# Optimization experiments

Measured on AMD Instinct MI355X. Metric: run time of the kernel, lower is better.

Reference implementation:

```python
import jax, jax.numpy as jnp
import numpy as np

N = 100000      # nodes
E = 3200000     # edges (before self-loops)
IN = 1          # input feature dim
H1, C = 4, 8    # layer1: 4 heads x 8 channels; layer2: 1 head x 8 channels
NEG_SLOPE = 0.2


def setup_inputs() -> dict:
    key = jax.random.key(0)
    ks = jax.random.split(key, 10)
    x = jax.random.normal(ks[0], (N, IN), jnp.float32)
    edge_index = jax.random.randint(ks[1], (2, E), 0, N, dtype=jnp.int32)
    # layer 1 params (GATConv(1, 8, heads=4))
    W1 = jax.random.normal(ks[2], (IN, H1 * C), jnp.float32) * 0.5
    a_src1 = jax.random.normal(ks[3], (H1, C), jnp.float32) * 0.5
    a_dst1 = jax.random.normal(ks[4], (H1, C), jnp.float32) * 0.5
    b1 = jnp.zeros((H1 * C,), jnp.float32)
    # layer 2 params (GATConv(32, 8, heads=1))
    W2 = jax.random.normal(ks[5], (H1 * C, C), jnp.float32) * 0.2
    a_src2 = jax.random.normal(ks[6], (1, C), jnp.float32) * 0.5
    a_dst2 = jax.random.normal(ks[7], (1, C), jnp.float32) * 0.5
    b2 = jnp.zeros((C,), jnp.float32)
    return {"x": x, "edge_index": edge_index, "W1": W1, "a_src1": a_src1,
            "a_dst1": a_dst1, "b1": b1, "W2": W2, "a_src2": a_src2,
            "a_dst2": a_dst2, "b2": b2}


def _gat_layer(x, src, dst, W, a_s, a_d, b, heads, ch):
    # Linear transform per head: [N, heads, ch]
    h = (x @ W).reshape(-1, heads, ch)
    # per-node attention logits
    al_s = jnp.einsum('nhc,hc->nh', h, a_s)  # [N, H]
    al_d = jnp.einsum('nhc,hc->nh', h, a_d)  # [N, H]
    # per-edge logits (message src -> dst)
    e = jax.nn.leaky_relu(al_s[src] + al_d[dst], NEG_SLOPE)  # [E', H]
    # segment softmax over incoming edges of each dst node
    m = jax.ops.segment_max(e, dst, num_segments=N)          # [N, H]
    e = jnp.exp(e - m[dst])
    s = jax.ops.segment_sum(e, dst, num_segments=N)          # [N, H]
    alpha = e / s[dst]                                       # [E', H]
    # weighted scatter-add aggregation
    out = jax.ops.segment_sum(h[src] * alpha[:, :, None], dst, num_segments=N)
    return out.reshape(N, heads * ch) + b


def reference(x, edge_index, W1, a_src1, a_dst1, b1, W2, a_src2, a_dst2, b2):
    loops = jnp.arange(N, dtype=edge_index.dtype)
    src = jnp.concatenate([edge_index[0], loops])  # add self-loops (PyG default)
    dst = jnp.concatenate([edge_index[1], loops])
    h = _gat_layer(x, src, dst, W1, a_src1, a_dst1, b1, H1, C)
    h = jax.nn.relu(h)
    out = _gat_layer(h, src, dst, W2, a_src2, a_dst2, b2, 1, C)
    return out
```

## Files before the change

kernel.cpp:

```cpp
#include <hip/hip_runtime.h>
#include <hip/hip_bf16.h>

#define NEG_SLOPE 0.2f
#define CAP   6144
#define CAPG  8192
#define CAPA  81920


__global__ void init_cc(int* __restrict__ curA, int* __restrict__ curB,
                        const float* __restrict__ W1,
                        const float* __restrict__ as1,
                        const float* __restrict__ ad1,
                        float* __restrict__ consts) {
    int t = threadIdx.x;
    if (t < 8) {
        int h = t & 3;
        const float* a = (t < 4) ? as1 : ad1;
        float s = 0.f;
        #pragma unroll
        for (int c = 0; c < 8; ++c)
            s += W1[h * 8 + c] * a[h * 8 + c];
        consts[t] = s;
    }
    if (t < 64) curA[t] = t * CAPA;
    curB[t] = t << 13;
}

__global__ void scatterA(const int* __restrict__ ei, int* __restrict__ curA,
                         unsigned int* __restrict__ bufA, int E) {
    __shared__ int cnt[64];
    __shared__ int basel[64];
    int t = threadIdx.x;
    int chunk = (E + gridDim.x - 1) / gridDim.x;
    int lo = blockIdx.x * chunk;
    int hi = min(E, lo + chunk);
    const int* dei = ei + E;
    if (t < 64) cnt[t] = 0;
    __syncthreads();
    bool vec = ((E & 3) == 0);
    int lo4 = (lo + 3) & ~3;
    int end4 = hi & ~3;
    if (vec && end4 > lo4) {
        for (int e = lo + t; e < lo4; e += 1024)
            atomicAdd(&cnt[dei[e] >> 11], 1);
        const int4* dei4 = (const int4*)dei;
        for (int v = (lo4 >> 2) + t; v < (end4 >> 2); v += 1024) {
            int4 d = dei4[v];
            atomicAdd(&cnt[d.x >> 11], 1);
            atomicAdd(&cnt[d.y >> 11], 1);
            atomicAdd(&cnt[d.z >> 11], 1);
            atomicAdd(&cnt[d.w >> 11], 1);
        }
        for (int e = end4 + t; e < hi; e += 1024)
            atomicAdd(&cnt[dei[e] >> 11], 1);
    } else {
        for (int e = lo + t; e < hi; e += 1024)
            atomicAdd(&cnt[dei[e] >> 11], 1);
    }
    __syncthreads();
    if (t < 64) {
        int c = cnt[t];
        basel[t] = c ? (atomicAdd(&curA[t], c) - t * CAPA) : 0;
        cnt[t] = 0;
    }
    __syncthreads();
    if (vec && end4 > lo4) {
        for (int e = lo + t; e < lo4; e += 1024) {
            int s = ei[e], d = dei[e];
            int sp = d >> 11;
            int off = basel[sp] + atomicAdd(&cnt[sp], 1);
            if (off < CAPA) bufA[sp * CAPA + off] = (unsigned)s | ((unsigned)(d & 2047) << 17);
        }
        const int4* sei4 = (const int4*)ei;
        const int4* dei4 = (const int4*)dei;
        for (int v = (lo4 >> 2) + t; v < (end4 >> 2); v += 1024) {
            int4 sv = sei4[v];
            int4 dv = dei4[v];
            int s0 = dv.x >> 11, s1 = dv.y >> 11, s2 = dv.z >> 11, s3 = dv.w >> 11;
            int o0 = basel[s0] + atomicAdd(&cnt[s0], 1);
            if (o0 < CAPA) bufA[s0 * CAPA + o0] = (unsigned)sv.x | ((unsigned)(dv.x & 2047) << 17);
            int o1 = basel[s1] + atomicAdd(&cnt[s1], 1);
            if (o1 < CAPA) bufA[s1 * CAPA + o1] = (unsigned)sv.y | ((unsigned)(dv.y & 2047) << 17);
            int o2 = basel[s2] + atomicAdd(&cnt[s2], 1);
            if (o2 < CAPA) bufA[s2 * CAPA + o2] = (unsigned)sv.z | ((unsigned)(dv.z & 2047) << 17);
            int o3 = basel[s3] + atomicAdd(&cnt[s3], 1);
            if (o3 < CAPA) bufA[s3 * CAPA + o3] = (unsigned)sv.w | ((unsigned)(dv.w & 2047) << 17);
        }
        for (int e = end4 + t; e < hi; e += 1024) {
            int s = ei[e], d = dei[e];
            int sp = d >> 11;
            int off = basel[sp] + atomicAdd(&cnt[sp], 1);
            if (off < CAPA) bufA[sp * CAPA + off] = (unsigned)s | ((unsigned)(d & 2047) << 17);
        }
    } else {
        for (int e = lo + t; e < hi; e += 1024) {
            int s = ei[e], d = dei[e];
            int sp = d >> 11;
            int off = basel[sp] + atomicAdd(&cnt[sp], 1);
            if (off < CAPA) bufA[sp * CAPA + off] = (unsigned)s | ((unsigned)(d & 2047) << 17);
        }
    }
}

__global__ void scatterB(const int* __restrict__ curA, int* __restrict__ curB,
                         const unsigned int* __restrict__ bufA,
                         unsigned int* __restrict__ pairs) {
    __shared__ int cnt[16];
    __shared__ int basel[16];
    int t = threadIdx.x;
    int sp = blockIdx.x >> 3;
    int part = blockIdx.x & 7;
    int base = sp * CAPA;
    int fill = min(curA[sp] - base, CAPA);
    if (fill <= 0) return;
    int lo = (fill * part) >> 3;
    int hi = (fill * (part + 1)) >> 3;
    for (int c0 = lo; c0 < hi; c0 += 8192) {
        int cend = min(hi, c0 + 8192);
        if (t < 16) cnt[t] = 0;
        __syncthreads();
        for (int i = c0 + t; i < cend; i += 1024)
            atomicAdd(&cnt[(bufA[base + i] >> 24) & 15], 1);
        __syncthreads();
        if (t < 16) {
            int c = cnt[t];
            int bkg = (sp << 4) + t;
            basel[t] = c ? (atomicAdd(&curB[bkg], c) - (bkg << 13)) : 0;
            cnt[t] = 0;
        }
        __syncthreads();
        for (int i = c0 + t; i < cend; i += 1024) {
            unsigned p = bufA[base + i];
            int b16 = (p >> 24) & 15;
            int off = basel[b16] + atomicAdd(&cnt[b16], 1);
            if (off < CAPG) {
                int bkg = (sp << 4) + b16;
                pairs[(bkg << 13) + off] = p & 0x00FFFFFFu;
            }
        }
        __syncthreads();
    }
}

__global__ __launch_bounds__(1024, 8)
void l1_comb(const float* __restrict__ x,
             const int* __restrict__ curB,
             const unsigned int* __restrict__ pairs,
             const float* __restrict__ consts,
             const float* __restrict__ W1, const float* __restrict__ b1,
             const float* __restrict__ W2,
             const float* __restrict__ as2, const float* __restrict__ ad2,
             float* __restrict__ h2, float* __restrict__ als2,
             float* __restrict__ ald2, int N) {
    __shared__ unsigned sbuf[CAP];
    __shared__ int hcnt[128], offs[128], hcur[128];
    __shared__ float xl[128];
    int t = threadIdx.x;
    int bk = blockIdx.x;
    int node0 = bk << 7;
    int nw = min(128, N - node0);
    if (t < 128) xl[t] = (t < nw) ? x[node0 + t] : 0.f;
    float S[4], D[4];
    #pragma unroll
    for (int h = 0; h < 4; ++h) { S[h] = consts[h]; D[h] = consts[4 + h]; }
    int base = bk << 13;
    int cnt_total = min(curB[bk] - base, CAPG);
    int g = t >> 3, j = t & 7;
    float sacc[4] = {0.f, 0.f, 0.f, 0.f};
    float tacc[4] = {0.f, 0.f, 0.f, 0.f};
    __syncthreads();
    float xd = xl[g];
    for (int c0 = 0; c0 < cnt_total; c0 += CAP) {
        int clen = min(CAP, cnt_total - c0);
        unsigned pr[6];
        #pragma unroll
        for (int k = 0; k < 6; ++k) {
            int idx = t + (k << 10);
            pr[k] = (idx < clen) ? pairs[base + c0 + idx] : 0xFFFFFFFFu;
        }
        if (t < 128) hcnt[t] = 0;
        __syncthreads();
        #pragma unroll
        for (int k = 0; k < 6; ++k)
            if (pr[k] != 0xFFFFFFFFu) atomicAdd(&hcnt[pr[k] >> 17], 1);
        __syncthreads();
        if (t < 64) {
            int h0 = hcnt[2 * t], h1 = hcnt[2 * t + 1];
            int s = h0 + h1, sc_ = s;
            #pragma unroll
            for (int o = 1; o < 64; o <<= 1) {
                int u = __shfl_up(sc_, o);
                if (t >= o) sc_ += u;
            }
            int excl = sc_ - s;
            offs[2 * t] = excl;          hcur[2 * t] = excl;
            offs[2 * t + 1] = excl + h0; hcur[2 * t + 1] = excl + h0;
        }
        __syncthreads();
        #pragma unroll
        for (int k = 0; k < 6; ++k)
            if (pr[k] != 0xFFFFFFFFu) {
                int loc = atomicAdd(&hcur[pr[k] >> 17], 1);
                sbuf[loc] = pr[k];
            }
        __syncthreads();
        int st = offs[g], en = st + hcnt[g];
        int i = st + j;
        float xs0 = 0.f, xs1 = 0.f;
        if (i < en) xs0 = x[sbuf[i] & 131071u];
        if (i + 8 < en) xs1 = x[sbuf[i + 8] & 131071u];
        for (; i < en; i += 8) {
            float xs = xs0;
            xs0 = xs1;
            int i2 = i + 16;
            xs1 = (i2 < en) ? x[sbuf[i2] & 131071u] : 0.f;
            #pragma unroll
            for (int h = 0; h < 4; ++h) {
                float v = xs * S[h] + xd * D[h];
                v = (v > 0.f) ? v : NEG_SLOPE * v;
                float w = __expf(v);
                sacc[h] += w;
                tacc[h] = fmaf(w, xs, tacc[h]);
            }
        }
        __syncthreads();
    }
    #pragma unroll
    for (int h = 0; h < 4; ++h) {
        sacc[h] += __shfl_xor(sacc[h], 1); sacc[h] += __shfl_xor(sacc[h], 2);
        sacc[h] += __shfl_xor(sacc[h], 4);
        tacc[h] += __shfl_xor(tacc[h], 1); tacc[h] += __shfl_xor(tacc[h], 2);
        tacc[h] += __shfl_xor(tacc[h], 4);
    }
    if (j == 0 && g < nw) {
        int n = node0 + g;
        float xn = xd;
        float o[8];
        #pragma unroll
        for (int c = 0; c < 8; ++c) o[c] = 0.f;
        #pragma unroll
        for (int h = 0; h < 4; ++h) {
            float v = xn * (S[h] + D[h]);
            v = (v > 0.f) ? v : NEG_SLOPE * v;
            float ww = __expf(v);
            float s1 = ww + sacc[h];
            float t1 = ww * xn + tacc[h];
            float tt = t1 / s1;
            #pragma unroll
            for (int c = 0; c < 8; ++c) {
                float rr = fmaxf(tt * W1[h * 8 + c] + b1[h * 8 + c], 0.f);
                #pragma unroll
                for (int c2 = 0; c2 < 8; ++c2) o[c2] += rr * W2[(h * 8 + c) * 8 + c2];
            }
        }
        float as = 0.f, ad = 0.f;
        #pragma unroll
        for (int c = 0; c < 8; ++c) { as += o[c] * as2[c]; ad += o[c] * ad2[c]; }
        float4* hv = (float4*)&h2[(size_t)n * 8];
        hv[0] = make_float4(o[0], o[1], o[2], o[3]);
        hv[1] = make_float4(o[4], o[5], o[6], o[7]);
        als2[n] = as;
        ald2[n] = ad;
    }
}

__global__ __launch_bounds__(1024, 8)
void l2_comb(const int* __restrict__ curB,
             const unsigned int* __restrict__ pairs,
             const float* __restrict__ als2, const float* __restrict__ ald2,
             const float* __restrict__ h2, const float* __restrict__ b2,
             float* __restrict__ out, int N) {
    __shared__ unsigned sbuf[CAP];
    __shared__ int hcnt[128], offs[128], hcur[128];
    __shared__ float adl[128];
    int t = threadIdx.x;
    int bk = blockIdx.x;
    int node0 = bk << 7;
    int nw = min(128, N - node0);
    if (t < 128) adl[t] = (t < nw) ? ald2[node0 + t] : 0.f;
    int base = bk << 13;
    int cnt_total = min(curB[bk] - base, CAPG);
    int g = t >> 3, j = t & 7;
    float acc[9];
    #pragma unroll
    for (int c = 0; c < 9; ++c) acc[c] = 0.f;
    __syncthreads();
    float adv = adl[g];
    for (int c0 = 0; c0 < cnt_total; c0 += CAP) {
        int clen = min(CAP, cnt_total - c0);
        unsigned pr[6];
        #pragma unroll
        for (int k = 0; k < 6; ++k) {
            int idx = t + (k << 10);
            pr[k] = (idx < clen) ? pairs[base + c0 + idx] : 0xFFFFFFFFu;
        }
        if (t < 128) hcnt[t] = 0;
        __syncthreads();
        #pragma unroll
        for (int k = 0; k < 6; ++k)
            if (pr[k] != 0xFFFFFFFFu) atomicAdd(&hcnt[pr[k] >> 17], 1);
        __syncthreads();
        if (t < 64) {
            int h0 = hcnt[2 * t], h1 = hcnt[2 * t + 1];
            int s = h0 + h1, sc_ = s;
            #pragma unroll
            for (int o = 1; o < 64; o <<= 1) {
                int u = __shfl_up(sc_, o);
                if (t >= o) sc_ += u;
            }
            int excl = sc_ - s;
            offs[2 * t] = excl;          hcur[2 * t] = excl;
            offs[2 * t + 1] = excl + h0; hcur[2 * t + 1] = excl + h0;
        }
        __syncthreads();
        #pragma unroll
        for (int k = 0; k < 6; ++k)
            if (pr[k] != 0xFFFFFFFFu) {
                int loc = atomicAdd(&hcur[pr[k] >> 17], 1);
                sbuf[loc] = pr[k];
            }
        __syncthreads();
        int st = offs[g], en = st + hcnt[g];
        int i = st + j;
        float a0 = 0.f, a1 = 0.f;
        float4 hA0 = make_float4(0,0,0,0), hB0 = hA0, hA1 = hA0, hB1 = hA0;
        if (i < en) {
            int s0 = (int)(sbuf[i] & 131071u);
            a0 = als2[s0];
            const float4* q = (const float4*)&h2[(size_t)s0 * 8];
            hA0 = q[0]; hB0 = q[1];
        }
        if (i + 8 < en) {
            int s1 = (int)(sbuf[i + 8] & 131071u);
            a1 = als2[s1];
            const float4* q = (const float4*)&h2[(size_t)s1 * 8];
            hA1 = q[0]; hB1 = q[1];
        }
        for (; i < en; i += 8) {
            float a = a0; float4 hA = hA0, hB = hB0;
            a0 = a1; hA0 = hA1; hB0 = hB1;
            int i2 = i + 16;
            if (i2 < en) {
                int s2 = (int)(sbuf[i2] & 131071u);
                a1 = als2[s2];
                const float4* q = (const float4*)&h2[(size_t)s2 * 8];
                hA1 = q[0]; hB1 = q[1];
            } else {
                a1 = 0.f;
            }
            float v = a + adv;
            v = (v > 0.f) ? v : NEG_SLOPE * v;
            float w = __expf(v);
            acc[0] += w;
            acc[1] = fmaf(w, hA.x, acc[1]); acc[2] = fmaf(w, hA.y, acc[2]);
            acc[3] = fmaf(w, hA.z, acc[3]); acc[4] = fmaf(w, hA.w, acc[4]);
            acc[5] = fmaf(w, hB.x, acc[5]); acc[6] = fmaf(w, hB.y, acc[6]);
            acc[7] = fmaf(w, hB.z, acc[7]); acc[8] = fmaf(w, hB.w, acc[8]);
        }
        __syncthreads();
    }
    #pragma unroll
    for (int c = 0; c < 9; ++c) {
        acc[c] += __shfl_xor(acc[c], 1);
        acc[c] += __shfl_xor(acc[c], 2);
        acc[c] += __shfl_xor(acc[c], 4);
    }
    if (j == 0 && g < nw) {
        int n = node0 + g;
        float v = als2[n] + adv;
        v = (v > 0.f) ? v : NEG_SLOPE * v;
        float ww = __expf(v);
        const float4* hv = (const float4*)&h2[(size_t)n * 8];
        float4 ha0 = hv[0], hb0 = hv[1];
        float s2v = acc[0] + ww;
        float inv = 1.f / s2v;
        float4* ov = (float4*)&out[(size_t)n * 8];
        ov[0] = make_float4((acc[1] + ww * ha0.x) * inv + b2[0],
                            (acc[2] + ww * ha0.y) * inv + b2[1],
                            (acc[3] + ww * ha0.z) * inv + b2[2],
                            (acc[4] + ww * ha0.w) * inv + b2[3]);
        ov[1] = make_float4((acc[5] + ww * hb0.x) * inv + b2[4],
                            (acc[6] + ww * hb0.y) * inv + b2[5],
                            (acc[7] + ww * hb0.z) * inv + b2[6],
                            (acc[8] + ww * hb0.w) * inv + b2[7]);
    }
}


__global__ void prep_consts(const float* __restrict__ W1,
                            const float* __restrict__ as1,
                            const float* __restrict__ ad1,
                            float* __restrict__ consts) {
    int t = threadIdx.x;
    if (t >= 8) return;
    int h = t & 3;
    const float* a = (t < 4) ? as1 : ad1;
    float s = 0.f;
    #pragma unroll
    for (int c = 0; c < 8; ++c)
        s += W1[h * 8 + c] * a[h * 8 + c];
    consts[t] = s;
}

__global__ void edge_pass1(const int* __restrict__ ei, const float* __restrict__ x,
                           const float* __restrict__ consts,
                           float* __restrict__ s1, float* __restrict__ t1, int E, int N) {
    int e = blockIdx.x * blockDim.x + threadIdx.x;
    if (e >= E + N) return;
    int src, dst;
    if (e < E) { src = ei[e]; dst = ei[E + e]; }
    else       { src = dst = e - E; }
    float xs = x[src], xd = x[dst];
    #pragma unroll
    for (int h = 0; h < 4; ++h) {
        float v = xs * consts[h] + xd * consts[4 + h];
        v = (v > 0.f) ? v : NEG_SLOPE * v;
        float w = __expf(v);
        atomicAdd(&s1[dst * 4 + h], w);
        atomicAdd(&t1[dst * 4 + h], w * xs);
    }
}

__global__ void node_mid(const float* __restrict__ s1, const float* __restrict__ t1,
                         const float* __restrict__ W1, const float* __restrict__ b1,
                         const float* __restrict__ W2,
                         const float* __restrict__ as2, const float* __restrict__ ad2,
                         float* __restrict__ h2, float* __restrict__ als2,
                         float* __restrict__ ald2, int N) {
    int n = blockIdx.x * blockDim.x + threadIdx.x;
    if (n >= N) return;
    float o[8];
    #pragma unroll
    for (int c = 0; c < 8; ++c) o[c] = 0.f;
    #pragma unroll
    for (int h = 0; h < 4; ++h) {
        float t = t1[n * 4 + h] / s1[n * 4 + h];
        #pragma unroll
        for (int c = 0; c < 8; ++c) {
            float r = fmaxf(t * W1[h * 8 + c] + b1[h * 8 + c], 0.f);
            #pragma unroll
            for (int c2 = 0; c2 < 8; ++c2) o[c2] += r * W2[(h * 8 + c) * 8 + c2];
        }
    }
    float as = 0.f, ad = 0.f;
    #pragma unroll
    for (int c = 0; c < 8; ++c) { h2[n * 8 + c] = o[c]; as += o[c] * as2[c]; ad += o[c] * ad2[c]; }
    als2[n] = as; ald2[n] = ad;
}

__global__ void edge_pass2(const int* __restrict__ ei, const float* __restrict__ als2,
                           const float* __restrict__ ald2, const float* __restrict__ h2,
                           float* __restrict__ s2, float* __restrict__ acc2, int E, int N) {
    int e = blockIdx.x * blockDim.x + threadIdx.x;
    if (e >= E + N) return;
    int src, dst;
    if (e < E) { src = ei[e]; dst = ei[E + e]; }
    else       { src = dst = e - E; }
    float v = als2[src] + ald2[dst];
    v = (v > 0.f) ? v : NEG_SLOPE * v;
    float w = __expf(v);
    atomicAdd(&s2[dst], w);
    const float4* hs = (const float4*)&h2[src * 8];
    float4 a = hs[0], bq = hs[1];
    float* acc = &acc2[dst * 8];
    atomicAdd(&acc[0], w * a.x);  atomicAdd(&acc[1], w * a.y);
    atomicAdd(&acc[2], w * a.z);  atomicAdd(&acc[3], w * a.w);
    atomicAdd(&acc[4], w * bq.x); atomicAdd(&acc[5], w * bq.y);
    atomicAdd(&acc[6], w * bq.z); atomicAdd(&acc[7], w * bq.w);
}

__global__ void node_out(const float* __restrict__ s2, const float* __restrict__ acc2,
                         const float* __restrict__ b2, float* __restrict__ out, int N) {
    int i = blockIdx.x * blockDim.x + threadIdx.x;
    if (i >= N * 8) return;
    out[i] = acc2[i] / s2[i >> 3] + b2[i & 7];
}


extern "C" void kernel_launch(void* const* d_in, const int* in_sizes, int n_in,
                              void* d_out, int out_size, void* d_ws, size_t ws_size,
                              hipStream_t stream) {
    const float* x   = (const float*)d_in[0];
    const int*   ei  = (const int*)d_in[1];
    const float* W1  = (const float*)d_in[2];
    const float* as1 = (const float*)d_in[3];
    const float* ad1 = (const float*)d_in[4];
    const float* b1  = (const float*)d_in[5];
    const float* W2  = (const float*)d_in[6];
    const float* as2 = (const float*)d_in[7];
    const float* ad2 = (const float*)d_in[8];
    const float* b2  = (const float*)d_in[9];
    float* out = (float*)d_out;

    const int N = in_sizes[0];
    const int E = in_sizes[1] / 2;
    const int NBK = (N + 127) >> 7;

    float* ws = (float*)d_ws;
    size_t need = (size_t)(16 + 64 + 1024 + 10 * (size_t)N
                           + (size_t)1024 * CAPG + (size_t)64 * CAPA) * sizeof(float);

    if (N <= 131072 && ws_size >= need) {
        float*    consts = ws;
        int*      curA   = (int*)(ws + 16);
        int*      curB   = curA + 64;
        float*    als2   = ws + 16 + 64 + 1024;
        float*    ald2   = als2 + N;
        float*    h2     = ald2 + N;
        unsigned* pairs  = (unsigned*)(h2 + 8 * (size_t)N);
        unsigned* bufA   = pairs + (size_t)1024 * CAPG;

        init_cc<<<1, 1024, 0, stream>>>(curA, curB, W1, as1, ad1, consts);
        scatterA<<<256, 1024, 0, stream>>>(ei, curA, bufA, E);
        scatterB<<<512, 1024, 0, stream>>>(curA, curB, bufA, pairs);
        l1_comb<<<NBK, 1024, 0, stream>>>(x, curB, pairs, consts,
                                          W1, b1, W2, as2, ad2, h2, als2, ald2, N);
        l2_comb<<<NBK, 1024, 0, stream>>>(curB, pairs, als2, ald2, h2, b2, out, N);
    } else {
        float* consts = ws;
        float* s1   = ws + 16;
        float* t1   = s1 + 4 * (size_t)N;
        float* h2   = t1 + 4 * (size_t)N;
        float* als2 = h2 + 8 * (size_t)N;
        float* ald2 = als2 + (size_t)N;
        float* s2   = ald2 + (size_t)N;
        float* acc2 = s2 + (size_t)N;

        hipMemsetAsync(ws, 0, (16 + 8 * (size_t)N) * sizeof(float), stream);
        hipMemsetAsync(s2, 0, 9 * (size_t)N * sizeof(float), stream);
        prep_consts<<<1, 64, 0, stream>>>(W1, as1, ad1, consts);
        int total = E + N;
        edge_pass1<<<(total + 255) / 256, 256, 0, stream>>>(ei, x, consts, s1, t1, E, N);
        node_mid<<<(N + 255) / 256, 256, 0, stream>>>(s1, t1, W1, b1, W2, as2, ad2, h2, als2, ald2, N);
        edge_pass2<<<(total + 255) / 256, 256, 0, stream>>>(ei, als2, ald2, h2, s2, acc2, E, N);
        node_out<<<(N * 8 + 255) / 256, 256, 0, stream>>>(s2, acc2, b2, out, N);
    }
}
```

Before: 201.5 us.

## Persist per-block sorted edge lists from layer 1 and reuse in layer 2

Layer 1 now sorts each 128-node bucket's edges by destination in shared memory once, writes the sorted list and per-node offset/count metadata to global memory, and layer 2 reads that layout directly instead of redoing the histogram, scan and shared-memory sort. Layer 2 also changes its work mapping: each of the 8 lanes per node now handles one output channel and walks all of that node's edges, rather than splitting edges across lanes and reducing with shuffles. This removes duplicated sorting work and barriers in layer 2. It costs extra global writes and reads of the sorted buffer plus larger workspace, and each lane now issues its own per-edge gathers of als2 and h2.

```diff
diff --git a/kernel.cpp b/kernel.cpp
--- a/kernel.cpp
+++ b/kernel.cpp
@@ -2,9 +2,9 @@
 #include <hip/hip_bf16.h>
 
 #define NEG_SLOPE 0.2f
-#define CAP   6144
-#define CAPG  8192
-#define CAPA  81920
+#define CAPS 8192
+#define CAPG 8192
+#define CAPA 81920
 
 
 __global__ void init_cc(int* __restrict__ curA, int* __restrict__ curB,
@@ -41,21 +41,16 @@
     int lo4 = (lo + 3) & ~3;
     int end4 = hi & ~3;
     if (vec && end4 > lo4) {
-        for (int e = lo + t; e < lo4; e += 1024)
-            atomicAdd(&cnt[dei[e] >> 11], 1);
+        for (int e = lo + t; e < lo4; e += 1024) atomicAdd(&cnt[dei[e] >> 11], 1);
         const int4* dei4 = (const int4*)dei;
         for (int v = (lo4 >> 2) + t; v < (end4 >> 2); v += 1024) {
             int4 d = dei4[v];
-            atomicAdd(&cnt[d.x >> 11], 1);
-            atomicAdd(&cnt[d.y >> 11], 1);
-            atomicAdd(&cnt[d.z >> 11], 1);
-            atomicAdd(&cnt[d.w >> 11], 1);
-        }
-        for (int e = end4 + t; e < hi; e += 1024)
-            atomicAdd(&cnt[dei[e] >> 11], 1);
+            atomicAdd(&cnt[d.x >> 11], 1); atomicAdd(&cnt[d.y >> 11], 1);
+            atomicAdd(&cnt[d.z >> 11], 1); atomicAdd(&cnt[d.w >> 11], 1);
+        }
+        for (int e = end4 + t; e < hi; e += 1024) atomicAdd(&cnt[dei[e] >> 11], 1);
     } else {
-        for (int e = lo + t; e < hi; e += 1024)
-            atomicAdd(&cnt[dei[e] >> 11], 1);
+        for (int e = lo + t; e < hi; e += 1024) atomicAdd(&cnt[dei[e] >> 11], 1);
     }
     __syncthreads();
     if (t < 64) {
@@ -66,16 +61,14 @@
     __syncthreads();
     if (vec && end4 > lo4) {
         for (int e = lo + t; e < lo4; e += 1024) {
-            int s = ei[e], d = dei[e];
-            int sp = d >> 11;
+            int s = ei[e], d = dei[e]; int sp = d >> 11;
             int off = basel[sp] + atomicAdd(&cnt[sp], 1);
             if (off < CAPA) bufA[sp * CAPA + off] = (unsigned)s | ((unsigned)(d & 2047) << 17);
         }
         const int4* sei4 = (const int4*)ei;
         const int4* dei4 = (const int4*)dei;
         for (int v = (lo4 >> 2) + t; v < (end4 >> 2); v += 1024) {
-            int4 sv = sei4[v];
-            int4 dv = dei4[v];
+            int4 sv = sei4[v]; int4 dv = dei4[v];
             int s0 = dv.x >> 11, s1 = dv.y >> 11, s2 = dv.z >> 11, s3 = dv.w >> 11;
             int o0 = basel[s0] + atomicAdd(&cnt[s0], 1);
             if (o0 < CAPA) bufA[s0 * CAPA + o0] = (unsigned)sv.x | ((unsigned)(dv.x & 2047) << 17);
@@ -87,15 +80,13 @@
             if (o3 < CAPA) bufA[s3 * CAPA + o3] = (unsigned)sv.w | ((unsigned)(dv.w & 2047) << 17);
         }
         for (int e = end4 + t; e < hi; e += 1024) {
-            int s = ei[e], d = dei[e];
-            int sp = d >> 11;
+            int s = ei[e], d = dei[e]; int sp = d >> 11;
             int off = basel[sp] + atomicAdd(&cnt[sp], 1);
             if (off < CAPA) bufA[sp * CAPA + off] = (unsigned)s | ((unsigned)(d & 2047) << 17);
         }
     } else {
         for (int e = lo + t; e < hi; e += 1024) {
-            int s = ei[e], d = dei[e];
-            int sp = d >> 11;
+            int s = ei[e], d = dei[e]; int sp = d >> 11;
             int off = basel[sp] + atomicAdd(&cnt[sp], 1);
             if (off < CAPA) bufA[sp * CAPA + off] = (unsigned)s | ((unsigned)(d & 2047) << 17);
         }
@@ -133,10 +124,7 @@
             unsigned p = bufA[base + i];
             int b16 = (p >> 24) & 15;
             int off = basel[b16] + atomicAdd(&cnt[b16], 1);
-            if (off < CAPG) {
-                int bkg = (sp << 4) + b16;
-                pairs[(bkg << 13) + off] = p & 0x00FFFFFFu;
-            }
+            if (off < CAPG) pairs[(((sp << 4) + b16) << 13) + off] = p & 0x00FFFFFFu;
         }
         __syncthreads();
     }
@@ -146,13 +134,14 @@
 void l1_comb(const float* __restrict__ x,
              const int* __restrict__ curB,
              const unsigned int* __restrict__ pairs,
+             unsigned int* __restrict__ gsorted, int* __restrict__ bmeta,
              const float* __restrict__ consts,
              const float* __restrict__ W1, const float* __restrict__ b1,
              const float* __restrict__ W2,
              const float* __restrict__ as2, const float* __restrict__ ad2,
              float* __restrict__ h2, float* __restrict__ als2,
              float* __restrict__ ald2, int N) {
-    __shared__ unsigned sbuf[CAP];
+    __shared__ unsigned sbuf[CAPS];
     __shared__ int hcnt[128], offs[128], hcur[128];
     __shared__ float xl[128];
     int t = threadIdx.x;
@@ -164,66 +153,71 @@
     #pragma unroll
     for (int h = 0; h < 4; ++h) { S[h] = consts[h]; D[h] = consts[4 + h]; }
     int base = bk << 13;
-    int cnt_total = min(curB[bk] - base, CAPG);
-    int g = t >> 3, j = t & 7;
+    int clen = min(curB[bk] - base, CAPG);
+    int clen6 = min(clen, 6144);
+    int g = t >> 3, jj = t & 7;
+    unsigned pr[6];
+    #pragma unroll
+    for (int k = 0; k < 6; ++k) {
+        int idx = t + (k << 10);
+        pr[k] = (idx < clen6) ? pairs[base + idx] : 0xFFFFFFFFu;
+    }
+    if (t < 128) hcnt[t] = 0;
+    __syncthreads();
+    #pragma unroll
+    for (int k = 0; k < 6; ++k)
+        if (pr[k] != 0xFFFFFFFFu) atomicAdd(&hcnt[pr[k] >> 17], 1);
+    for (int idx = 6144 + t; idx < clen; idx += 1024)
+        atomicAdd(&hcnt[pairs[base + idx] >> 17], 1);
+    __syncthreads();
+    if (t < 64) {
+        int h0 = hcnt[2 * t], h1 = hcnt[2 * t + 1];
+        int s = h0 + h1, sc_ = s;
+        #pragma unroll
+        for (int o = 1; o < 64; o <<= 1) {
+            int u = __shfl_up(sc_, o);
+            if (t >= o) sc_ += u;
+        }
+        int excl = sc_ - s;
+        offs[2 * t] = excl;          hcur[2 * t] = excl;
+        offs[2 * t + 1] = excl + h0; hcur[2 * t + 1] = excl + h0;
+    }
+    __syncthreads();
+    #pragma unroll
+    for (int k = 0; k < 6; ++k)
+        if (pr[k] != 0xFFFFFFFFu) {
+            int loc = atomicAdd(&hcur[pr[k] >> 17], 1);
+            sbuf[loc] = pr[k];
+        }
+    for (int idx = 6144 + t; idx < clen; idx += 1024) {
+        unsigned p = pairs[base + idx];
+        int loc = atomicAdd(&hcur[p >> 17], 1);
+        sbuf[loc] = p;
+    }
+    __syncthreads();
+    for (int i = t; i < clen; i += 1024) gsorted[base + i] = sbuf[i];
+    if (t < 128) bmeta[(bk << 7) + t] = offs[t] | (hcnt[t] << 14);
+    float xd = xl[g];
     float sacc[4] = {0.f, 0.f, 0.f, 0.f};
     float tacc[4] = {0.f, 0.f, 0.f, 0.f};
-    __syncthreads();
-    float xd = xl[g];
-    for (int c0 = 0; c0 < cnt_total; c0 += CAP) {
-        int clen = min(CAP, cnt_total - c0);
-        unsigned pr[6];
-        #pragma unroll
-        for (int k = 0; k < 6; ++k) {
-            int idx = t + (k << 10);
-            pr[k] = (idx < clen) ? pairs[base + c0 + idx] : 0xFFFFFFFFu;
-        }
-        if (t < 128) hcnt[t] = 0;
-        __syncthreads();
-        #pragma unroll
-        for (int k = 0; k < 6; ++k)
-            if (pr[k] != 0xFFFFFFFFu) atomicAdd(&hcnt[pr[k] >> 17], 1);
-        __syncthreads();
-        if (t < 64) {
-            int h0 = hcnt[2 * t], h1 = hcnt[2 * t + 1];
-            int s = h0 + h1, sc_ = s;
-            #pragma unroll
-            for (int o = 1; o < 64; o <<= 1) {
-                int u = __shfl_up(sc_, o);
-                if (t >= o) sc_ += u;
-            }
-            int excl = sc_ - s;
-            offs[2 * t] = excl;          hcur[2 * t] = excl;
-            offs[2 * t + 1] = excl + h0; hcur[2 * t + 1] = excl + h0;
-        }
-        __syncthreads();
-        #pragma unroll
-        for (int k = 0; k < 6; ++k)
-            if (pr[k] != 0xFFFFFFFFu) {
-                int loc = atomicAdd(&hcur[pr[k] >> 17], 1);
-                sbuf[loc] = pr[k];
-            }
-        __syncthreads();
-        int st = offs[g], en = st + hcnt[g];
-        int i = st + j;
-        float xs0 = 0.f, xs1 = 0.f;
-        if (i < en) xs0 = x[sbuf[i] & 131071u];
-        if (i + 8 < en) xs1 = x[sbuf[i + 8] & 131071u];
-        for (; i < en; i += 8) {
-            float xs = xs0;
-            xs0 = xs1;
-            int i2 = i + 16;
-            xs1 = (i2 < en) ? x[sbuf[i2] & 131071u] : 0.f;
-            #pragma unroll
-            for (int h = 0; h < 4; ++h) {
-                float v = xs * S[h] + xd * D[h];
-                v = (v > 0.f) ? v : NEG_SLOPE * v;
-                float w = __expf(v);
-                sacc[h] += w;
-                tacc[h] = fmaf(w, xs, tacc[h]);
-            }
-        }
-        __syncthreads();
+    int st = offs[g], en = st + hcnt[g];
+    int i = st + jj;
+    float xs0 = 0.f, xs1 = 0.f;
+    if (i < en) xs0 = x[sbuf[i] & 131071u];
+    if (i + 8 < en) xs1 = x[sbuf[i + 8] & 131071u];
+    for (; i < en; i += 8) {
+        float xs = xs0;
+        xs0 = xs1;
+        int i2 = i + 16;
+        xs1 = (i2 < en) ? x[sbuf[i2] & 131071u] : 0.f;
+        #pragma unroll
+        for (int h = 0; h < 4; ++h) {
+            float v = xs * S[h] + xd * D[h];
+            v = (v > 0.f) ? v : NEG_SLOPE * v;
+            float w = __expf(v);
+            sacc[h] += w;
+            tacc[h] = fmaf(w, xs, tacc[h]);
+        }
     }
     #pragma unroll
     for (int h = 0; h < 4; ++h) {
@@ -232,7 +226,7 @@
         tacc[h] += __shfl_xor(tacc[h], 1); tacc[h] += __shfl_xor(tacc[h], 2);
         tacc[h] += __shfl_xor(tacc[h], 4);
     }
-    if (j == 0 && g < nw) {
+    if (jj == 0 && g < nw) {
         int n = node0 + g;
         float xn = xd;
         float o[8];
@@ -264,126 +258,54 @@
     }
 }
 
-__global__ __launch_bounds__(1024, 8)
-void l2_comb(const int* __restrict__ curB,
-             const unsigned int* __restrict__ pairs,
+__global__ __launch_bounds__(1024)
+void l2_comb(const unsigned int* __restrict__ gsorted,
+             const int* __restrict__ bmeta,
              const float* __restrict__ als2, const float* __restrict__ ald2,
              const float* __restrict__ h2, const float* __restrict__ b2,
              float* __restrict__ out, int N) {
-    __shared__ unsigned sbuf[CAP];
-    __shared__ int hcnt[128], offs[128], hcur[128];
     __shared__ float adl[128];
     int t = threadIdx.x;
     int bk = blockIdx.x;
     int node0 = bk << 7;
     int nw = min(128, N - node0);
     if (t < 128) adl[t] = (t < nw) ? ald2[node0 + t] : 0.f;
+    __syncthreads();
+    int g = t >> 3, j = t & 7;
+    if (g >= nw) return;
     int base = bk << 13;
-    int cnt_total = min(curB[bk] - base, CAPG);
-    int g = t >> 3, j = t & 7;
-    float acc[9];
-    #pragma unroll
-    for (int c = 0; c < 9; ++c) acc[c] = 0.f;
-    __syncthreads();
+    int pk = bmeta[(bk << 7) + g];
+    int st = pk & 16383, cgn = pk >> 14;
+    const unsigned* run = gsorted + base + st;
     float adv = adl[g];
-    for (int c0 = 0; c0 < cnt_total; c0 += CAP) {
-        int clen = min(CAP, cnt_total - c0);
-        unsigned pr[6];
-        #pragma unroll
-        for (int k = 0; k < 6; ++k) {
-            int idx = t + (k << 10);
-            pr[k] = (idx < clen) ? pairs[base + c0 + idx] : 0xFFFFFFFFu;
-        }
-        if (t < 128) hcnt[t] = 0;
-        __syncthreads();
-        #pragma unroll
-        for (int k = 0; k < 6; ++k)
-            if (pr[k] != 0xFFFFFFFFu) atomicAdd(&hcnt[pr[k] >> 17], 1);
-        __syncthreads();
-        if (t < 64) {
-            int h0 = hcnt[2 * t], h1 = hcnt[2 * t + 1];
-            int s = h0 + h1, sc_ = s;
-            #pragma unroll
-            for (int o = 1; o < 64; o <<= 1) {
-                int u = __shfl_up(sc_, o);
-                if (t >= o) sc_ += u;
-            }
-            int excl = sc_ - s;
-            offs[2 * t] = excl;          hcur[2 * t] = excl;
-            offs[2 * t + 1] = excl + h0; hcur[2 * t + 1] = excl + h0;
-        }
-        __syncthreads();
-        #pragma unroll
-        for (int k = 0; k < 6; ++k)
-            if (pr[k] != 0xFFFFFFFFu) {
-                int loc = atomicAdd(&hcur[pr[k] >> 17], 1);
-                sbuf[loc] = pr[k];
-            }
-        __syncthreads();
-        int st = offs[g], en = st + hcnt[g];
-        int i = st + j;
-        float a0 = 0.f, a1 = 0.f;
-        float4 hA0 = make_float4(0,0,0,0), hB0 = hA0, hA1 = hA0, hB1 = hA0;
-        if (i < en) {
-            int s0 = (int)(sbuf[i] & 131071u);
-            a0 = als2[s0];
-            const float4* q = (const float4*)&h2[(size_t)s0 * 8];
-            hA0 = q[0]; hB0 = q[1];
-        }
-        if (i + 8 < en) {
-            int s1 = (int)(sbuf[i + 8] & 131071u);
-            a1 = als2[s1];
-            const float4* q = (const float4*)&h2[(size_t)s1 * 8];
-            hA1 = q[0]; hB1 = q[1];
-        }
-        for (; i < en; i += 8) {
-            float a = a0; float4 hA = hA0, hB = hB0;
-            a0 = a1; hA0 = hA1; hB0 = hB1;
-            int i2 = i + 16;
-            if (i2 < en) {
-                int s2 = (int)(sbuf[i2] & 131071u);
-                a1 = als2[s2];
-                const float4* q = (const float4*)&h2[(size_t)s2 * 8];
-                hA1 = q[0]; hB1 = q[1];
-            } else {
-                a1 = 0.f;
-            }
-            float v = a + adv;
-            v = (v > 0.f) ? v : NEG_SLOPE * v;
-            float w = __expf(v);
-            acc[0] += w;
-            acc[1] = fmaf(w, hA.x, acc[1]); acc[2] = fmaf(w, hA.y, acc[2]);
-            acc[3] = fmaf(w, hA.z, acc[3]); acc[4] = fmaf(w, hA.w, acc[4]);
-            acc[5] = fmaf(w, hB.x, acc[5]); acc[6] = fmaf(w, hB.y, acc[6]);
-            acc[7] = fmaf(w, hB.z, acc[7]); acc[8] = fmaf(w, hB.w, acc[8]);
-        }
-        __syncthreads();
-    }
-    #pragma unroll
-    for (int c = 0; c < 9; ++c) {
-        acc[c] += __shfl_xor(acc[c], 1);
-        acc[c] += __shfl_xor(acc[c], 2);
-        acc[c] += __shfl_xor(acc[c], 4);
-    }
-    if (j == 0 && g < nw) {
-        int n = node0 + g;
-        float v = als2[n] + adv;
+    float accv = 0.f, sw = 0.f;
+    float a0 = 0.f, h0 = 0.f, a1 = 0.f, h1 = 0.f;
+    unsigned p2 = 0u;
+    if (cgn > 0) { int s = (int)(run[0] & 131071u); a0 = als2[s]; h0 = h2[(size_t)s * 8 + j]; }
+    if (cgn > 1) { int s = (int)(run[1] & 131071u); a1 = als2[s]; h1 = h2[(size_t)s * 8 + j]; }
+    if (cgn > 2) p2 = run[2];
+    for (int i = 0; i < cgn; ++i) {
+        float v = a0 + adv;
         v = (v > 0.f) ? v : NEG_SLOPE * v;
-        float ww = __expf(v);
-        const float4* hv = (const float4*)&h2[(size_t)n * 8];
-        float4 ha0 = hv[0], hb0 = hv[1];
-        float s2v = acc[0] + ww;
-        float inv = 1.f / s2v;
-        float4* ov = (float4*)&out[(size_t)n * 8];
-        ov[0] = make_float4((acc[1] + ww * ha0.x) * inv + b2[0],
-                            (acc[2] + ww * ha0.y) * inv + b2[1],
-                            (acc[3] + ww * ha0.z) * inv + b2[2],
-                            (acc[4] + ww * ha0.w) * inv + b2[3]);
-        ov[1] = make_float4((acc[5] + ww * hb0.x) * inv + b2[4],
-                            (acc[6] + ww * hb0.y) * inv + b2[5],
-                            (acc[7] + ww * hb0.z) * inv + b2[6],
-                            (acc[8] + ww * hb0.w) * inv + b2[7]);
-    }
+        float w = __expf(v);
+        sw += w;
+        accv = fmaf(w, h0, accv);
+        a0 = a1; h0 = h1;
+        int i2 = i + 2;
+        if (i2 < cgn) {
+            int s = (int)(p2 & 131071u);
+            a1 = als2[s];
+            h1 = h2[(size_t)s * 8 + j];
+        }
+        p2 = (i + 3 < cgn) ? run[i + 3] : 0u;
+    }
+    int n = node0 + g;
+    float v = als2[n] + adv;
+    v = (v > 0.f) ? v : NEG_SLOPE * v;
+    float ww = __expf(v);
+    float hs = h2[(size_t)n * 8 + j];
+    float s2v = sw + ww;
+    out[(size_t)n * 8 + j] = (accv + ww * hs) / s2v + b2[j];
 }
 
 
@@ -497,25 +419,27 @@
     const int NBK = (N + 127) >> 7;
 
     float* ws = (float*)d_ws;
-    size_t need = (size_t)(16 + 64 + 1024 + 10 * (size_t)N
-                           + (size_t)1024 * CAPG + (size_t)64 * CAPA) * sizeof(float);
+    size_t need = ((size_t)16 + 64 + 1024 + 131072 + 10 * (size_t)N
+                   + 2 * (size_t)1024 * CAPG + (size_t)64 * CAPA) * sizeof(float);
 
     if (N <= 131072 && ws_size >= need) {
-        float*    consts = ws;
-        int*      curA   = (int*)(ws + 16);
-        int*      curB   = curA + 64;
-        float*    als2   = ws + 16 + 64 + 1024;
-        float*    ald2   = als2 + N;
-        float*    h2     = ald2 + N;
-        unsigned* pairs  = (unsigned*)(h2 + 8 * (size_t)N);
-        unsigned* bufA   = pairs + (size_t)1024 * CAPG;
+        float*    consts  = ws;
+        int*      curA    = (int*)(ws + 16);
+        int*      curB    = curA + 64;
+        int*      bmeta   = curB + 1024;
+        float*    als2    = (float*)(bmeta + 131072);
+        float*    ald2    = als2 + N;
+        float*    h2      = ald2 + N;
+        unsigned* pairs   = (unsigned*)(h2 + 8 * (size_t)N);
+        unsigned* gsorted = pairs + (size_t)1024 * CAPG;
+        unsigned* bufA    = gsorted + (size_t)1024 * CAPG;
 
         init_cc<<<1, 1024, 0, stream>>>(curA, curB, W1, as1, ad1, consts);
         scatterA<<<256, 1024, 0, stream>>>(ei, curA, bufA, E);
         scatterB<<<512, 1024, 0, stream>>>(curA, curB, bufA, pairs);
-        l1_comb<<<NBK, 1024, 0, stream>>>(x, curB, pairs, consts,
+        l1_comb<<<NBK, 1024, 0, stream>>>(x, curB, pairs, gsorted, bmeta, consts,
                                           W1, b1, W2, as2, ad2, h2, als2, ald2, N);
-        l2_comb<<<NBK, 1024, 0, stream>>>(curB, pairs, als2, ald2, h2, b2, out, N);
+        l2_comb<<<NBK, 1024, 0, stream>>>(gsorted, bmeta, als2, ald2, h2, b2, out, N);
     } else {
         float* consts = ws;
         float* s1   = ws + 16;
```

Measured after the change: 209.7 us. 4.1% more time.
